# Kernel tuning notes

Measured on AMD Instinct MI355X. Metric: run time of the kernel, lower is better.

## Reference

```python
import math
import jax, jax.numpy as jnp
import numpy as np

DIMS = 20
MULT = 8
K = (DIMS + 1) * MULT  # 168 mixture components
N = 524288
EPS = 1.0              # log_density default eps
BASE_COV = 0.1
LOG_NORM = -DIMS / 2 * math.log(2 * math.pi)


def setup_inputs() -> dict:
    key = jax.random.key(0)
    k1, k2, k3 = jax.random.split(key, 3)
    sample = jax.random.normal(k1, (N, DIMS), dtype=jnp.float32) * 0.3
    alpha = jax.random.normal(k2, (K,), dtype=jnp.float32) * 0.1
    mu = jax.random.uniform(k3, (K, DIMS), dtype=jnp.float32, minval=-0.5, maxval=0.5)
    cov = jnp.full((K, DIMS), BASE_COV, dtype=jnp.float32)
    return {"sample": sample, "alpha": alpha, "mu": mu, "cov": cov}


def reference(sample, alpha, mu, cov):
    # Faithful vectorization of the per-component Python loop in log_density.
    var = EPS ** 2
    weights = jax.nn.softmax(alpha)                       # [K]
    i = jnp.arange(K) // MULT                             # component group index, 0..DIMS
    d = jnp.arange(DIMS)
    # cov[:i] *= var  ->  scale first i dims of each component's cov by var
    scale = jnp.where(d[None, :] < i[:, None], var, 1.0)  # [K, D]
    inv = 1.0 / (cov * scale)                             # [K, D]
    # det_cov = var**i * (1/10)**(dims - i)  (exactly as in the source)
    fi = i.astype(jnp.float32)
    det_cov = var ** fi * BASE_COV ** (DIMS - fi)         # [K]
    sig_term = det_cov ** -0.5                            # [K]
    # quad[n,k] = sum_d (x[n,d]-mu[k,d])^2 * inv[k,d], expanded into GEMMs
    quad = (sample ** 2) @ inv.T \
           - 2.0 * (sample @ (mu * inv).T) \
           + jnp.sum(mu * mu * inv, axis=1)[None, :]      # [N, K]
    results = sig_term * jnp.exp(-0.5 * quad) * weights   # [N, K]
    density = results.sum(axis=1, keepdims=True)          # [N, 1]
    return jnp.log(density) + LOG_NORM
```

## Files before the change

### kernel.cpp

```cpp
#include <hip/hip_runtime.h>
#include <math.h>


#define DIMS     20
#define MULT     8
#define K_COMP   168
#define KC_PAD   176
#define BROW     72
#define BASE_COV 0.1f
#define LOG2E    1.4426950408889634f
#define LN2      0.6931471805599453f
#define LOG_NORM -18.378770664093453f
#define CPW      8
#define NB       1024

typedef _Float16 f16x8 __attribute__((ext_vector_type(8)));
typedef _Float16 f16x2 __attribute__((ext_vector_type(2)));
typedef float    f32x4 __attribute__((ext_vector_type(4)));
typedef unsigned int uint;
typedef uint u32x4 __attribute__((ext_vector_type(4)));

__device__ __forceinline__ uint pk(float lo, float hi) {
    return __builtin_bit_cast(uint, __builtin_amdgcn_cvt_pkrtz(lo, hi));
}
__device__ __forceinline__ uint pksq(uint a) {
    f16x2 v = __builtin_bit_cast(f16x2, a);
    return __builtin_bit_cast(uint, (f16x2)(v * v));
}

__global__ __launch_bounds__(256) void gm_fused(const float* __restrict__ sample,
                                                const float* __restrict__ alpha,
                                                const float* __restrict__ mu,
                                                const float* __restrict__ cov,
                                                float* __restrict__ out) {
    __shared__ __attribute__((aligned(16))) _Float16 lds_T[KC_PAD][BROW];
    __shared__ float sh_logZ;
    const int tid = threadIdx.x;

    uint* bz = (uint*)&lds_T[0][0];
    for (int i = tid; i < KC_PAD * BROW / 2; i += 256) bz[i] = 0u;
    __syncthreads();

    if (tid < 64) {
        float a0 = (tid       < K_COMP) ? alpha[tid]       : -1e30f;
        float a1 = (tid + 64  < K_COMP) ? alpha[tid + 64]  : -1e30f;
        float a2 = (tid + 128 < K_COMP) ? alpha[tid + 128] : -1e30f;
        float m = fmaxf(fmaxf(a0, a1), a2);
        for (int msk = 32; msk; msk >>= 1) m = fmaxf(m, __shfl_xor(m, msk, 64));
        float s = __expf(a0 - m) + __expf(a1 - m) + __expf(a2 - m);
        for (int msk = 32; msk; msk >>= 1) s += __shfl_xor(s, msk, 64);
        if (tid == 0) sh_logZ = m + __logf(s);
    }
    __syncthreads();

    if (tid < K_COMP) {
        const int   n  = tid;
        const int   i  = n / MULT;
        const float fi = (float)i;
        const float var = 1.0f;
        float logdet = fi * __logf(var) + ((float)DIMS - fi) * __logf(BASE_COV);
        const float4* cvp = (const float4*)(cov + n * DIMS);
        const float4* mup = (const float4*)(mu + n * DIMS);
        float4 c0 = cvp[0], c1 = cvp[1], c2 = cvp[2], c3 = cvp[3], c4 = cvp[4];
        float4 m0 = mup[0], m1 = mup[1], m2 = mup[2], m3 = mup[3], m4 = mup[4];
        float C = 0.0f;
        auto emit = [&](int d, float cc, float mm) {
            float scale = (d < i) ? var : 1.0f;
            float inv   = 1.0f / (cc * scale);
            C += mm * mm * inv;
            lds_T[n][d]        = (_Float16)(-0.5f * inv * LOG2E);
            lds_T[n][DIMS + d] = (_Float16)(mm * inv * LOG2E);
        };
        emit( 0, c0.x, m0.x); emit( 1, c0.y, m0.y); emit( 2, c0.z, m0.z); emit( 3, c0.w, m0.w);
        emit( 4, c1.x, m1.x); emit( 5, c1.y, m1.y); emit( 6, c1.z, m1.z); emit( 7, c1.w, m1.w);
        emit( 8, c2.x, m2.x); emit( 9, c2.y, m2.y); emit(10, c2.z, m2.z); emit(11, c2.w, m2.w);
        emit(12, c3.x, m3.x); emit(13, c3.y, m3.y); emit(14, c3.z, m3.z); emit(15, c3.w, m3.w);
        emit(16, c4.x, m4.x); emit(17, c4.y, m4.y); emit(18, c4.z, m4.z); emit(19, c4.w, m4.w);
        float L2 = ((alpha[n] - sh_logZ) - 0.5f * logdet - 0.5f * C) * LOG2E;
        lds_T[n][2 * DIMS] = (_Float16)L2;
    } else if (tid < KC_PAD) {
        lds_T[tid][2 * DIMS] = (_Float16)(-65504.0f);
    }
    __syncthreads();

    const int w = tid >> 6, l = tid & 63, q = l >> 4, c = l & 15;
    const bool qa = (q & 1) != 0, qb = (q & 2) != 0;
    const uint onezero = 0x00003C00u;
    const f32x4 zero = { 0.f, 0.f, 0.f, 0.f };
    const int base = blockIdx.x * (64 * CPW) + w * 16;

    const float4* rp = (const float4*)(sample + (size_t)(base + c) * DIMS);
    float4 r0 = rp[0], r1 = rp[1], r2 = rp[2], r3 = rp[3], r4 = rp[4];

    for (int cc = 0; cc < CPW; ++cc) {
        const int rb = base + cc * 64;
        float4 n0 = r0, n1 = r1, n2 = r2, n3 = r3, n4 = r4;
        if (cc + 1 < CPW) {
            const float4* np = (const float4*)(sample + (size_t)(rb + 64 + c) * DIMS);
            n0 = np[0]; n1 = np[1]; n2 = np[2]; n3 = np[3]; n4 = np[4];
        }

        uint q0 = pk(r0.x, r0.y), q1 = pk(r0.z, r0.w);
        uint q2 = pk(r1.x, r1.y), q3 = pk(r1.z, r1.w);
        uint q4 = pk(r2.x, r2.y), q5 = pk(r2.z, r2.w);
        uint q6 = pk(r3.x, r3.y), q7 = pk(r3.z, r3.w);
        uint q8 = pk(r4.x, r4.y), q9 = pk(r4.z, r4.w);
        uint s0 = pksq(q0), s1 = pksq(q1), s2 = pksq(q2), s3 = pksq(q3), s4 = pksq(q4);
        uint s5 = pksq(q5), s6 = pksq(q6), s7 = pksq(q7), s8 = pksq(q8), s9 = pksq(q9);

        uint f1_0 = qb ? (qa ? q2 : s8) : (qa ? s4 : s0);
        uint f1_1 = qb ? (qa ? q3 : s9) : (qa ? s5 : s1);
        uint f1_2 = qb ? (qa ? q4 : q0) : (qa ? s6 : s2);
        uint f1_3 = qb ? (qa ? q5 : q1) : (qa ? s7 : s3);
        uint f2_0 = qb ? 0u : (qa ? onezero : q6);
        uint f2_1 = qb ? 0u : (qa ? 0u : q7);
        uint f2_2 = qb ? 0u : (qa ? 0u : q8);
        uint f2_3 = qb ? 0u : (qa ? 0u : q9);
        u32x4 w1 = { f1_0, f1_1, f1_2, f1_3 };
        u32x4 w2 = { f2_0, f2_1, f2_2, f2_3 };
        f16x8 sf1 = __builtin_bit_cast(f16x8, w1);
        f16x8 sf2 = __builtin_bit_cast(f16x8, w2);

        float dens0 = 0.0f, dens1 = 0.0f;
#pragma unroll
        for (int t = 0; t < KC_PAD / 16; ++t) {
            f16x8 cf1 = *(const f16x8*)&lds_T[t * 16 + c][q * 8];
            f16x8 cf2 = *(const f16x8*)&lds_T[t * 16 + c][32 + q * 8];
            f32x4 acc = __builtin_amdgcn_mfma_f32_16x16x32_f16(cf1, sf1, zero, 0, 0, 0);
            acc       = __builtin_amdgcn_mfma_f32_16x16x32_f16(cf2, sf2, acc,  0, 0, 0);
            dens0 += __builtin_amdgcn_exp2f(acc[0]) + __builtin_amdgcn_exp2f(acc[1]);
            dens1 += __builtin_amdgcn_exp2f(acc[2]) + __builtin_amdgcn_exp2f(acc[3]);
        }
        float dens = dens0 + dens1;
        dens += __shfl_xor(dens, 16, 64);
        dens += __shfl_xor(dens, 32, 64);
        if (l < 16)
            out[rb + l] = LN2 * __builtin_amdgcn_logf(dens) + LOG_NORM;

        r0 = n0; r1 = n1; r2 = n2; r3 = n3; r4 = n4;
    }
}

extern "C" void kernel_launch(void* const* d_in, const int* in_sizes, int n_in,
                              void* d_out, int out_size, void* d_ws, size_t ws_size,
                              hipStream_t stream) {
    const float* sample = (const float*)d_in[0];
    const float* alpha  = (const float*)d_in[1];
    const float* mu     = (const float*)d_in[2];
    const float* cov    = (const float*)d_in[3];
    float* out = (float*)d_out;
    gm_fused<<<NB, 256, 0, stream>>>(sample, alpha, mu, cov, out);
}
```

Measured before the change: 99.55 us.

## Interchange loops so each LDS component fragment feeds all eight row chunks

All eight row chunks' sample fragments are loaded and packed up front. The loop over component tiles becomes the outer loop, so each pair of LDS fragment reads is reused across eight independent MFMA chains instead of being reloaded per chunk. This cuts LDS traffic eightfold and gives the scheduler independent MFMA/exp work to interleave. In exchange it raises register pressure (eight fragment pairs plus eight accumulators) and issues all global loads at once rather than software-pipelining them, which may lower occupancy.

```diff
diff --git a/kernel.cpp b/kernel.cpp
--- a/kernel.cpp
+++ b/kernel.cpp
@@ -87,58 +87,68 @@
     const bool qa = (q & 1) != 0, qb = (q & 2) != 0;
     const uint onezero = 0x00003C00u;
     const f32x4 zero = { 0.f, 0.f, 0.f, 0.f };
-    const int base = blockIdx.x * (64 * CPW) + w * 16;
+    const int base = blockIdx.x * (64 * CPW) + w * 16 + c;
 
-    const float4* rp = (const float4*)(sample + (size_t)(base + c) * DIMS);
-    float4 r0 = rp[0], r1 = rp[1], r2 = rp[2], r3 = rp[3], r4 = rp[4];
+#define MAKE_FRAGS(CC)                                                          \
+    f16x8 sf1_##CC, sf2_##CC;                                                   \
+    {                                                                           \
+        const float4* rp = (const float4*)(sample + (size_t)(base + (CC) * 64) * DIMS); \
+        float4 r0 = rp[0], r1 = rp[1], r2 = rp[2], r3 = rp[3], r4 = rp[4];      \
+        uint q0 = pk(r0.x, r0.y), q1 = pk(r0.z, r0.w);                          \
+        uint q2 = pk(r1.x, r1.y), q3 = pk(r1.z, r1.w);                          \
+        uint q4 = pk(r2.x, r2.y), q5 = pk(r2.z, r2.w);                          \
+        uint q6 = pk(r3.x, r3.y), q7 = pk(r3.z, r3.w);                          \
+        uint q8 = pk(r4.x, r4.y), q9 = pk(r4.z, r4.w);                          \
+        uint s0 = pksq(q0), s1 = pksq(q1), s2 = pksq(q2), s3 = pksq(q3);        \
+        uint s4 = pksq(q4), s5 = pksq(q5), s6 = pksq(q6), s7 = pksq(q7);        \
+        uint s8 = pksq(q8), s9 = pksq(q9);                                      \
+        uint f1_0 = qb ? (qa ? q2 : s8) : (qa ? s4 : s0);                       \
+        uint f1_1 = qb ? (qa ? q3 : s9) : (qa ? s5 : s1);                       \
+        uint f1_2 = qb ? (qa ? q4 : q0) : (qa ? s6 : s2);                       \
+        uint f1_3 = qb ? (qa ? q5 : q1) : (qa ? s7 : s3);                       \
+        uint f2_0 = qb ? 0u : (qa ? onezero : q6);                              \
+        uint f2_1 = qb ? 0u : (qa ? 0u : q7);                                   \
+        uint f2_2 = qb ? 0u : (qa ? 0u : q8);                                   \
+        uint f2_3 = qb ? 0u : (qa ? 0u : q9);                                   \
+        u32x4 w1 = { f1_0, f1_1, f1_2, f1_3 };                                  \
+        u32x4 w2 = { f2_0, f2_1, f2_2, f2_3 };                                  \
+        sf1_##CC = __builtin_bit_cast(f16x8, w1);                               \
+        sf2_##CC = __builtin_bit_cast(f16x8, w2);                               \
+    }
 
-    for (int cc = 0; cc < CPW; ++cc) {
-        const int rb = base + cc * 64;
-        float4 n0 = r0, n1 = r1, n2 = r2, n3 = r3, n4 = r4;
-        if (cc + 1 < CPW) {
-            const float4* np = (const float4*)(sample + (size_t)(rb + 64 + c) * DIMS);
-            n0 = np[0]; n1 = np[1]; n2 = np[2]; n3 = np[3]; n4 = np[4];
+    MAKE_FRAGS(0) MAKE_FRAGS(1) MAKE_FRAGS(2) MAKE_FRAGS(3)
+    MAKE_FRAGS(4) MAKE_FRAGS(5) MAKE_FRAGS(6) MAKE_FRAGS(7)
+#undef MAKE_FRAGS
+
+    float d0 = 0.f, d1 = 0.f, d2 = 0.f, d3 = 0.f;
+    float d4 = 0.f, d5 = 0.f, d6 = 0.f, d7 = 0.f;
+#pragma unroll
+    for (int t = 0; t < KC_PAD / 16; ++t) {
+        f16x8 cf1 = *(const f16x8*)&lds_T[t * 16 + c][q * 8];
+        f16x8 cf2 = *(const f16x8*)&lds_T[t * 16 + c][32 + q * 8];
+#define DO_CHUNK(CC)                                                            \
+        {                                                                       \
+            f32x4 acc = __builtin_amdgcn_mfma_f32_16x16x32_f16(cf1, sf1_##CC, zero, 0, 0, 0); \
+            acc       = __builtin_amdgcn_mfma_f32_16x16x32_f16(cf2, sf2_##CC, acc,  0, 0, 0); \
+            d##CC += (__builtin_amdgcn_exp2f(acc[0]) + __builtin_amdgcn_exp2f(acc[1]))        \
+                   + (__builtin_amdgcn_exp2f(acc[2]) + __builtin_amdgcn_exp2f(acc[3]));       \
         }
+        DO_CHUNK(0) DO_CHUNK(1) DO_CHUNK(2) DO_CHUNK(3)
+        DO_CHUNK(4) DO_CHUNK(5) DO_CHUNK(6) DO_CHUNK(7)
+#undef DO_CHUNK
+    }
 
-        uint q0 = pk(r0.x, r0.y), q1 = pk(r0.z, r0.w);
-        uint q2 = pk(r1.x, r1.y), q3 = pk(r1.z, r1.w);
-        uint q4 = pk(r2.x, r2.y), q5 = pk(r2.z, r2.w);
-        uint q6 = pk(r3.x, r3.y), q7 = pk(r3.z, r3.w);
-        uint q8 = pk(r4.x, r4.y), q9 = pk(r4.z, r4.w);
-        uint s0 = pksq(q0), s1 = pksq(q1), s2 = pksq(q2), s3 = pksq(q3), s4 = pksq(q4);
-        uint s5 = pksq(q5), s6 = pksq(q6), s7 = pksq(q7), s8 = pksq(q8), s9 = pksq(q9);
-
-        uint f1_0 = qb ? (qa ? q2 : s8) : (qa ? s4 : s0);
-        uint f1_1 = qb ? (qa ? q3 : s9) : (qa ? s5 : s1);
-        uint f1_2 = qb ? (qa ? q4 : q0) : (qa ? s6 : s2);
-        uint f1_3 = qb ? (qa ? q5 : q1) : (qa ? s7 : s3);
-        uint f2_0 = qb ? 0u : (qa ? onezero : q6);
-        uint f2_1 = qb ? 0u : (qa ? 0u : q7);
-        uint f2_2 = qb ? 0u : (qa ? 0u : q8);
-        uint f2_3 = qb ? 0u : (qa ? 0u : q9);
-        u32x4 w1 = { f1_0, f1_1, f1_2, f1_3 };
-        u32x4 w2 = { f2_0, f2_1, f2_2, f2_3 };
-        f16x8 sf1 = __builtin_bit_cast(f16x8, w1);
-        f16x8 sf2 = __builtin_bit_cast(f16x8, w2);
-
-        float dens0 = 0.0f, dens1 = 0.0f;
-#pragma unroll
-        for (int t = 0; t < KC_PAD / 16; ++t) {
-            f16x8 cf1 = *(const f16x8*)&lds_T[t * 16 + c][q * 8];
-            f16x8 cf2 = *(const f16x8*)&lds_T[t * 16 + c][32 + q * 8];
-            f32x4 acc = __builtin_amdgcn_mfma_f32_16x16x32_f16(cf1, sf1, zero, 0, 0, 0);
-            acc       = __builtin_amdgcn_mfma_f32_16x16x32_f16(cf2, sf2, acc,  0, 0, 0);
-            dens0 += __builtin_amdgcn_exp2f(acc[0]) + __builtin_amdgcn_exp2f(acc[1]);
-            dens1 += __builtin_amdgcn_exp2f(acc[2]) + __builtin_amdgcn_exp2f(acc[3]);
-        }
-        float dens = dens0 + dens1;
-        dens += __shfl_xor(dens, 16, 64);
-        dens += __shfl_xor(dens, 32, 64);
-        if (l < 16)
-            out[rb + l] = LN2 * __builtin_amdgcn_logf(dens) + LOG_NORM;
-
-        r0 = n0; r1 = n1; r2 = n2; r3 = n3; r4 = n4;
+    const int ob = blockIdx.x * (64 * CPW) + w * 16;
+#define FINISH(CC, DD)                                                          \
+    {                                                                           \
+        float dn = DD;                                                          \
+        dn += __shfl_xor(dn, 16, 64);                                           \
+        dn += __shfl_xor(dn, 32, 64);                                           \
+        if (l < 16) out[ob + (CC) * 64 + l] = LN2 * __builtin_amdgcn_logf(dn) + LOG_NORM; \
     }
+    FINISH(0, d0) FINISH(1, d1) FINISH(2, d2) FINISH(3, d3)
+    FINISH(4, d4) FINISH(5, d5) FINISH(6, d6) FINISH(7, d7)
+#undef FINISH
 }
 
 extern "C" void kernel_launch(void* const* d_in, const int* in_sizes, int n_in,
```

Result: slower. 115.4 us (+15.9%).
